# Kernel optimization log

Hardware: AMD Instinct MI355X
Metric: run time of the kernel (lower is better)

Reference implementation:

```python
import jax, jax.numpy as jnp
import numpy as np

D_MODEL = 1024
NHEAD = 16
HEAD_DIM = D_MODEL // NHEAD
B, S = 4, 2048


def setup_inputs() -> dict:
    key = jax.random.key(0)
    ks = jax.random.split(key, 10)
    scale = 1.0 / np.sqrt(D_MODEL)
    inp = {
        "x": jax.random.normal(ks[0], (B, S, D_MODEL), dtype=jnp.float32),
        "y": jax.random.normal(ks[1], (B, S, D_MODEL), dtype=jnp.float32),
        "wq": jax.random.normal(ks[2], (D_MODEL, D_MODEL), dtype=jnp.float32) * scale,
        "bq": jnp.zeros((D_MODEL,), dtype=jnp.float32),
        "wk": jax.random.normal(ks[3], (D_MODEL, D_MODEL), dtype=jnp.float32) * scale,
        "bk": jnp.zeros((D_MODEL,), dtype=jnp.float32),
        "wv": jax.random.normal(ks[4], (D_MODEL, D_MODEL), dtype=jnp.float32) * scale,
        "bv": jnp.zeros((D_MODEL,), dtype=jnp.float32),
        "wo": jax.random.normal(ks[5], (D_MODEL, D_MODEL), dtype=jnp.float32) * scale,
        "bo": jnp.zeros((D_MODEL,), dtype=jnp.float32),
    }
    return inp


def reference(x, y, wq, bq, wk, bk, wv, bv, wo, bo):
    # Linear projections (torch nn.Linear: x @ W.T + b; here weights stored as [in, out])
    q = x @ wq + bq  # [B, S, D]
    k = y @ wk + bk
    v = y @ wv + bv
    # split heads -> [B, H, S, Dh]
    def heads(t):
        return t.reshape(B, S, NHEAD, HEAD_DIM).transpose(0, 2, 1, 3)
    q, k, v = heads(q), heads(k), heads(v)
    scores = jnp.einsum("bhqd,bhkd->bhqk", q, k) / jnp.sqrt(jnp.float32(HEAD_DIM))
    attn = jax.nn.softmax(scores, axis=-1)  # dropout = identity in eval mode
    out = jnp.einsum("bhqk,bhkd->bhqd", attn, v)
    out = out.transpose(0, 2, 1, 3).reshape(B, S, D_MODEL)
    return out @ wo + bo
```

## Files before the change

kernel.cpp:

```cpp
#include <hip/hip_runtime.h>
#include <stdint.h>

#define D_MODEL 1024
#define NHEAD 16
#define HEAD_DIM 64
#define BATCH 4
#define SEQ 2048
#define ROWS (BATCH*SEQ)

typedef __attribute__((ext_vector_type(8))) short short8;
typedef __attribute__((ext_vector_type(4))) float f32x4;
typedef __attribute__((ext_vector_type(2))) unsigned int u32x2;
typedef unsigned short u16;
typedef unsigned int u32;

#define QSCALE 0.18033688011112042f

__device__ __forceinline__ u16 f2b(float f) {
  union { float f; uint32_t u; } in; in.f = f;
  uint32_t u = in.u;
  return (u16)((u + 0x7FFFu + ((u >> 16) & 1u)) >> 16);
}

__device__ __forceinline__ void async_lds16(const void* g, void* l) {
  __builtin_amdgcn_global_load_lds(
      (const __attribute__((address_space(1))) uint32_t*)g,
      (__attribute__((address_space(3))) uint32_t*)l,
      16, 0, 0);
}

__device__ __forceinline__ u32 pack_bf16(float lo, float hi) {
  union { float f; uint32_t u; } a, b; a.f = lo; b.f = hi;
  return __builtin_amdgcn_perm(b.u + 0x8000u, a.u + 0x8000u, 0x07060302u);
}

__global__ void __launch_bounds__(256) cvt_kernel(const float* __restrict__ x,
                                                  const float* __restrict__ y,
                                                  u16* __restrict__ xb,
                                                  u16* __restrict__ yb) {
  const float* in = blockIdx.y ? y : x;
  u16* out = blockIdx.y ? yb : xb;
  int i = blockIdx.x * 256 + threadIdx.x;
  float4 v = ((const float4*)in)[i];
  ushort4 o;
  o.x = f2b(v.x); o.y = f2b(v.y); o.z = f2b(v.z); o.w = f2b(v.w);
  ((ushort4*)out)[i] = o;
}

__global__ void __launch_bounds__(256) wtrans_kernel(const float* __restrict__ wq,
                                                     const float* __restrict__ wk,
                                                     const float* __restrict__ wv,
                                                     const float* __restrict__ wo,
                                                     u16* __restrict__ wtbase) {
  __shared__ u16 tile[64 * 65];
  int z = blockIdx.z;
  const float* w = (z == 0) ? wq : (z == 1 ? wk : (z == 2 ? wv : wo));
  u16* wt = wtbase + (size_t)z * D_MODEL * D_MODEL;
  int t = threadIdx.x;
  int c = t & 63, rb = t >> 6;
  int k0 = blockIdx.x * 64, n0 = blockIdx.y * 64;
#pragma unroll
  for (int i = 0; i < 16; ++i) {
    int r = rb + i * 4;
    tile[c * 65 + r] = f2b(w[(size_t)(k0 + r) * D_MODEL + n0 + c]);
  }
  __syncthreads();
#pragma unroll
  for (int i = 0; i < 16; ++i) {
    int r = rb + i * 4;
    wt[(size_t)(n0 + r) * D_MODEL + k0 + c] = tile[r * 65 + c];
  }
}

template <int MODE>
__device__ __forceinline__ void gemm_bt_core(const u16* __restrict__ A,
                                             const u16* __restrict__ Bt,
                                             const float* __restrict__ bias,
                                             void* __restrict__ Cout, float scale,
                                             int m0, int n0) {
  constexpr int K = 1024, N = 1024;
  constexpr bool SWAP = (MODE != 2);
  __shared__ u16 As[2][128 * 32];
  __shared__ u16 Bs[2][128 * 32];
  int tid = threadIdx.x;
  int wave = tid >> 6, lane = tid & 63;
  int quad = lane >> 4, l16 = lane & 15;
  int wm = wave & 1, wn = wave >> 1;

  f32x4 acc[4][4];
#pragma unroll
  for (int p = 0; p < 4; ++p)
#pragma unroll
    for (int q = 0; q < 4; ++q) acc[p][q] = f32x4{0.f, 0.f, 0.f, 0.f};

  int srow = lane >> 2;
  int scol = (lane & 3) * 16;

  for (int k0 = 0; k0 < K; k0 += 64) {
#pragma unroll
    for (int kh = 0; kh < 2; ++kh) {
#pragma unroll
      for (int i = 0; i < 2; ++i) {
        int c = wave * 2 + i;
        const char* ga = (const char*)(A + (size_t)(m0 + c * 16 + srow) * K + k0 + kh * 32) + scol;
        async_lds16(ga, (char*)As[kh] + c * 1024);
        const char* gb = (const char*)(Bt + (size_t)(n0 + c * 16 + srow) * K + k0 + kh * 32) + scol;
        async_lds16(gb, (char*)Bs[kh] + c * 1024);
      }
    }
    __syncthreads();

#pragma unroll
    for (int kh = 0; kh < 2; ++kh) {
      short8 fa[4], fb[4];
#pragma unroll
      for (int p = 0; p < 4; ++p)
        fa[p] = SWAP
          ? *(const short8*)(Bs[kh] + (wn * 64 + p * 16 + l16) * 32 + quad * 8)
          : *(const short8*)(As[kh] + (wm * 64 + p * 16 + l16) * 32 + quad * 8);
#pragma unroll
      for (int q = 0; q < 4; ++q)
        fb[q] = SWAP
          ? *(const short8*)(As[kh] + (wm * 64 + q * 16 + l16) * 32 + quad * 8)
          : *(const short8*)(Bs[kh] + (wn * 64 + q * 16 + l16) * 32 + quad * 8);
#pragma unroll
      for (int p = 0; p < 4; ++p)
#pragma unroll
        for (int q = 0; q < 4; ++q)
          acc[p][q] = __builtin_amdgcn_mfma_f32_16x16x32_bf16(fa[p], fb[q], acc[p][q], 0, 0, 0);
    }
    __syncthreads();
  }

  if (MODE == 2) {
    int sblk = n0 + wn * 64;
    int bb = sblk >> 11;
    int ssb = sblk & 2047;
#pragma unroll
    for (int p = 0; p < 4; ++p) {
      int dbase = m0 + wm * 64 + p * 16 + quad * 4;
      float4 b4 = *(const float4*)(bias + dbase);
#pragma unroll
      for (int r = 0; r < 4; ++r) {
        int d = dbase + r;
        float bv = ((const float*)&b4)[r];
        u32 lo = pack_bf16(acc[p][0][r] + bv, acc[p][1][r] + bv);
        u32 hi = pack_bf16(acc[p][2][r] + bv, acc[p][3][r] + bv);
        size_t vtrow = ((size_t)bb * 16 + (d >> 6)) * 64 + (d & 63);
        *(u32x2*)((u16*)Cout + vtrow * 2048 + ssb + 4 * l16) = u32x2{lo, hi};
      }
    }
  } else {
#pragma unroll
    for (int p = 0; p < 4; ++p) {
      int nbase = n0 + wn * 64 + p * 16 + quad * 4;
      float4 b4 = *(const float4*)(bias + nbase);
#pragma unroll
      for (int q = 0; q < 4; ++q) {
        size_t mrow = (size_t)(m0 + wm * 64 + q * 16 + l16);
        float v0 = (acc[p][q][0] + b4.x) * scale;
        float v1 = (acc[p][q][1] + b4.y) * scale;
        float v2 = (acc[p][q][2] + b4.z) * scale;
        float v3 = (acc[p][q][3] + b4.w) * scale;
        if (MODE == 1) {
          *(f32x4*)((float*)Cout + mrow * N + nbase) = f32x4{v0, v1, v2, v3};
        } else {
          *(u32x2*)((u16*)Cout + mrow * N + nbase) = u32x2{pack_bf16(v0, v1), pack_bf16(v2, v3)};
        }
      }
    }
  }
}

__global__ void __launch_bounds__(256, 4) gemm_qkv_kernel(
    const u16* __restrict__ xb, const u16* __restrict__ yb,
    const u16* __restrict__ wqT, const u16* __restrict__ wkT, const u16* __restrict__ wvT,
    const float* __restrict__ bq, const float* __restrict__ bk, const float* __restrict__ bv,
    u16* __restrict__ q, u16* __restrict__ k, u16* __restrict__ vt) {
  int bx = blockIdx.x, z = blockIdx.y;
  if (z == 0) {
    gemm_bt_core<0>(xb, wqT, bq, q, QSCALE, (bx >> 3) * 128, (bx & 7) * 128);
  } else if (z == 1) {
    gemm_bt_core<0>(yb, wkT, bk, k, 1.0f, (bx >> 3) * 128, (bx & 7) * 128);
  } else {
    gemm_bt_core<2>(wvT, yb, bv, vt, 1.0f, (bx & 7) * 128, (bx >> 3) * 128);
  }
}

__global__ void __launch_bounds__(256, 4) gemm_o_kernel(const u16* __restrict__ ao,
                                                        const u16* __restrict__ woT,
                                                        const float* __restrict__ bo,
                                                        float* __restrict__ out) {
  gemm_bt_core<1>(ao, woT, bo, out, 1.0f, blockIdx.y * 128, blockIdx.x * 128);
}

__global__ void __launch_bounds__(256, 4) attn_kernel(const u16* __restrict__ Q,
                                                      const u16* __restrict__ Kp,
                                                      const u16* __restrict__ Vt,
                                                      u16* __restrict__ Outp) {
  __shared__ u16 Ks[2][64 * 64];
  __shared__ u16 Vts[2][64 * 64];
  __shared__ u16 Ps[4][16 * 64];

  int tid = threadIdx.x, wave = tid >> 6, lane = tid & 63;
  int quad = lane >> 4, l16 = lane & 15;
  int bh = blockIdx.x;
  int b = bh >> 4, h = bh & 15;
  int q0 = blockIdx.y * 128 + wave * 32;
  size_t gbase = (size_t)b * SEQ * D_MODEL;
  const u16* kbase = Kp + gbase + (size_t)h * HEAD_DIM;
  const u16* vbase = Vt + (size_t)bh * HEAD_DIM * SEQ;
  const u16* qrow = Q + gbase + (size_t)q0 * D_MODEL + (size_t)h * HEAD_DIM;

  short8 aq[2][2];
#pragma unroll
  for (int rs = 0; rs < 2; ++rs)
#pragma unroll
    for (int dc = 0; dc < 2; ++dc)
      aq[rs][dc] = *(const short8*)(qrow + (size_t)(rs * 16 + l16) * D_MODEL + dc * 32 + quad * 8);

  f32x4 Oacc[2][4];
  float lpart[2][4];
#pragma unroll
  for (int rs = 0; rs < 2; ++rs)
#pragma unroll
    for (int ni = 0; ni < 4; ++ni) Oacc[rs][ni] = f32x4{0.f, 0.f, 0.f, 0.f};
#pragma unroll
  for (int rs = 0; rs < 2; ++rs)
#pragma unroll
    for (int r = 0; r < 4; ++r) lpart[rs][r] = 0.f;

  size_t koff[2], voff[2];
  int dstoff[2];
#pragma unroll
  for (int i = 0; i < 2; ++i) {
    int c = i * 256 + tid;
    int krow = c >> 3, kgp = c & 7;
    koff[i] = (size_t)krow * D_MODEL + (size_t)((kgp ^ (krow & 7)) * 8);
    voff[i] = (size_t)krow * SEQ + (size_t)((kgp ^ (krow & 7)) * 8);
    dstoff[i] = i * 4096 + wave * 1024;
  }

#pragma unroll
  for (int i = 0; i < 2; ++i) {
    async_lds16(kbase + koff[i], (char*)Ks[0] + dstoff[i]);
    async_lds16(vbase + voff[i], (char*)Vts[0] + dstoff[i]);
  }

  constexpr int NT = SEQ / 64;
  for (int t = 0; t < NT; ++t) {
    int cur = t & 1;
    __syncthreads();
    if (t + 1 < NT) {
      size_t kvoff = (size_t)(t + 1) * 64;
#pragma unroll
      for (int i = 0; i < 2; ++i) {
        async_lds16(kbase + kvoff * D_MODEL + koff[i], (char*)Ks[cur ^ 1] + dstoff[i]);
        async_lds16(vbase + kvoff + voff[i], (char*)Vts[cur ^ 1] + dstoff[i]);
      }
    }

    const u16* Kc = Ks[cur];
    const u16* Vc = Vts[cur];
    u16* Pw = Ps[wave];
    int x = l16 & 7;

    short8 kf[4][2];
#pragma unroll
    for (int sub = 0; sub < 4; ++sub) {
      const u16* kr = Kc + (sub * 16 + l16) * 64;
      kf[sub][0] = *(const short8*)(kr + ((quad ^ x) << 3));
      kf[sub][1] = *(const short8*)(kr + (((4 + quad) ^ x) << 3));
    }

    short8 pa[2][2];
#pragma unroll
    for (int rs = 0; rs < 2; ++rs) {
      f32x4 S[4];
#pragma unroll
      for (int sub = 0; sub < 4; ++sub) {
        f32x4 s = f32x4{0.f, 0.f, 0.f, 0.f};
        s = __builtin_amdgcn_mfma_f32_16x16x32_bf16(aq[rs][0], kf[sub][0], s, 0, 0, 0);
        s = __builtin_amdgcn_mfma_f32_16x16x32_bf16(aq[rs][1], kf[sub][1], s, 0, 0, 0);
        S[sub] = s;
      }
#pragma unroll
      for (int r = 0; r < 4; ++r) {
        float p0 = __builtin_amdgcn_exp2f(S[0][r]);
        float p1 = __builtin_amdgcn_exp2f(S[1][r]);
        float p2 = __builtin_amdgcn_exp2f(S[2][r]);
        float p3 = __builtin_amdgcn_exp2f(S[3][r]);
        lpart[rs][r] += (p0 + p1) + (p2 + p3);
        u32 lo = pack_bf16(p0, p1);
        u32 hi = pack_bf16(p2, p3);
        int row = quad * 4 + r;
        int off = row * 64 + (((l16 >> 1) ^ (row & 7)) << 3) + ((l16 & 1) << 2);
        *(u32x2*)(Pw + off) = u32x2{lo, hi};
      }
#pragma unroll
      for (int kc = 0; kc < 2; ++kc)
        pa[rs][kc] = *(const short8*)(Pw + l16 * 64 + ((((kc << 2) + quad) ^ x) << 3));
    }

#pragma unroll
    for (int kc = 0; kc < 2; ++kc) {
#pragma unroll
      for (int ni = 0; ni < 4; ++ni) {
        int d = ni * 16 + l16;
        short8 bv = *(const short8*)(Vc + d * 64 + ((((kc << 2) + quad) ^ (l16 & 7)) << 3));
        Oacc[0][ni] = __builtin_amdgcn_mfma_f32_16x16x32_bf16(pa[0][kc], bv, Oacc[0][ni], 0, 0, 0);
        Oacc[1][ni] = __builtin_amdgcn_mfma_f32_16x16x32_bf16(pa[1][kc], bv, Oacc[1][ni], 0, 0, 0);
      }
    }
  }

#pragma unroll
  for (int rs = 0; rs < 2; ++rs)
#pragma unroll
    for (int r = 0; r < 4; ++r) {
      float l = lpart[rs][r];
      l += __shfl_xor(l, 1);
      l += __shfl_xor(l, 2);
      l += __shfl_xor(l, 4);
      l += __shfl_xor(l, 8);
      float inv = 1.0f / l;
      size_t orow = gbase + (size_t)(q0 + rs * 16 + quad * 4 + r) * D_MODEL + (size_t)h * HEAD_DIM;
#pragma unroll
      for (int ni = 0; ni < 4; ++ni)
        Outp[orow + ni * 16 + l16] = f2b(Oacc[rs][ni][r] * inv);
    }
}

extern "C" void kernel_launch(void* const* d_in, const int* in_sizes, int n_in,
                              void* d_out, int out_size, void* d_ws, size_t ws_size,
                              hipStream_t stream) {
  const float* x  = (const float*)d_in[0];
  const float* y  = (const float*)d_in[1];
  const float* wq = (const float*)d_in[2];
  const float* bq = (const float*)d_in[3];
  const float* wk = (const float*)d_in[4];
  const float* bk = (const float*)d_in[5];
  const float* wv = (const float*)d_in[6];
  const float* bv = (const float*)d_in[7];
  const float* wo = (const float*)d_in[8];
  const float* bo = (const float*)d_in[9];
  float* out = (float*)d_out;

  char* ws = (char*)d_ws;
  const size_t SZ_ACT = (size_t)ROWS * D_MODEL * 2;
  const size_t SZ_W   = (size_t)D_MODEL * D_MODEL * 2;
  u16* xb  = (u16*)(ws);
  u16* yb  = (u16*)(ws + SZ_ACT);
  u16* wT  = (u16*)(ws + 2 * SZ_ACT);
  u16* wqT = wT;
  u16* wkT = (u16*)(ws + 2 * SZ_ACT + SZ_W);
  u16* wvT = (u16*)(ws + 2 * SZ_ACT + 2 * SZ_W);
  u16* woT = (u16*)(ws + 2 * SZ_ACT + 3 * SZ_W);
  u16* qb  = (u16*)(ws + 2 * SZ_ACT + 4 * SZ_W);
  u16* kb  = (u16*)(ws + 3 * SZ_ACT + 4 * SZ_W);
  u16* vt  = (u16*)(ws + 4 * SZ_ACT + 4 * SZ_W);
  u16* ao  = (u16*)(ws + 5 * SZ_ACT + 4 * SZ_W);

  cvt_kernel<<<dim3(8192, 2), 256, 0, stream>>>(x, y, xb, yb);
  wtrans_kernel<<<dim3(16, 16, 4), 256, 0, stream>>>(wq, wk, wv, wo, wT);
  gemm_qkv_kernel<<<dim3(512, 3), 256, 0, stream>>>(xb, yb, wqT, wkT, wvT, bq, bk, bv, qb, kb, vt);
  attn_kernel<<<dim3(64, 16), 256, 0, stream>>>(qb, kb, vt, ao);
  gemm_o_kernel<<<dim3(8, 64), 256, 0, stream>>>(ao, woT, bo, out);
}
```

Baseline: 327.6 us.

## Load GEMM and attention MFMA operands directly from global memory, drop LDS staging

Removes the async global-to-LDS double-buffered staging in both the projection GEMM core and the attention kernel. Each lane now reads its MFMA fragments straight from global memory through precomputed row pointers, which removes the __syncthreads barriers and the LDS traffic. In exchange, the reuse of tiles across waves is lost: each wave re-fetches the same K/V and A/B rows through the cache hierarchy, and load latency is no longer hidden by the double buffering. The P tile still goes through per-wave LDS.

```diff
diff --git a/kernel.cpp b/kernel.cpp
--- a/kernel.cpp
+++ b/kernel.cpp
@@ -20,13 +20,6 @@
   union { float f; uint32_t u; } in; in.f = f;
   uint32_t u = in.u;
   return (u16)((u + 0x7FFFu + ((u >> 16) & 1u)) >> 16);
-}
-
-__device__ __forceinline__ void async_lds16(const void* g, void* l) {
-  __builtin_amdgcn_global_load_lds(
-      (const __attribute__((address_space(1))) uint32_t*)g,
-      (__attribute__((address_space(3))) uint32_t*)l,
-      16, 0, 0);
 }
 
 __device__ __forceinline__ u32 pack_bf16(float lo, float hi) {
@@ -80,8 +73,6 @@
                                              int m0, int n0) {
   constexpr int K = 1024, N = 1024;
   constexpr bool SWAP = (MODE != 2);
-  __shared__ u16 As[2][128 * 32];
-  __shared__ u16 Bs[2][128 * 32];
   int tid = threadIdx.x;
   int wave = tid >> 6, lane = tid & 63;
   int quad = lane >> 4, l16 = lane & 15;
@@ -93,43 +84,31 @@
 #pragma unroll
     for (int q = 0; q < 4; ++q) acc[p][q] = f32x4{0.f, 0.f, 0.f, 0.f};
 
-  int srow = lane >> 2;
-  int scol = (lane & 3) * 16;
+  const u16* par[4];
+  const u16* pbr[4];
+#pragma unroll
+  for (int p = 0; p < 4; ++p) {
+    int arow = SWAP ? (n0 + wn * 64 + p * 16 + l16) : (m0 + wm * 64 + p * 16 + l16);
+    int brow = SWAP ? (m0 + wm * 64 + p * 16 + l16) : (n0 + wn * 64 + p * 16 + l16);
+    par[p] = (SWAP ? Bt : A) + (size_t)arow * K + quad * 8;
+    pbr[p] = (SWAP ? A : Bt) + (size_t)brow * K + quad * 8;
+  }
 
   for (int k0 = 0; k0 < K; k0 += 64) {
 #pragma unroll
     for (int kh = 0; kh < 2; ++kh) {
-#pragma unroll
-      for (int i = 0; i < 2; ++i) {
-        int c = wave * 2 + i;
-        const char* ga = (const char*)(A + (size_t)(m0 + c * 16 + srow) * K + k0 + kh * 32) + scol;
-        async_lds16(ga, (char*)As[kh] + c * 1024);
-        const char* gb = (const char*)(Bt + (size_t)(n0 + c * 16 + srow) * K + k0 + kh * 32) + scol;
-        async_lds16(gb, (char*)Bs[kh] + c * 1024);
-      }
-    }
-    __syncthreads();
-
-#pragma unroll
-    for (int kh = 0; kh < 2; ++kh) {
+      int ko = k0 + kh * 32;
       short8 fa[4], fb[4];
 #pragma unroll
-      for (int p = 0; p < 4; ++p)
-        fa[p] = SWAP
-          ? *(const short8*)(Bs[kh] + (wn * 64 + p * 16 + l16) * 32 + quad * 8)
-          : *(const short8*)(As[kh] + (wm * 64 + p * 16 + l16) * 32 + quad * 8);
-#pragma unroll
-      for (int q = 0; q < 4; ++q)
-        fb[q] = SWAP
-          ? *(const short8*)(As[kh] + (wm * 64 + q * 16 + l16) * 32 + quad * 8)
-          : *(const short8*)(Bs[kh] + (wn * 64 + q * 16 + l16) * 32 + quad * 8);
+      for (int p = 0; p < 4; ++p) fa[p] = *(const short8*)(par[p] + ko);
+#pragma unroll
+      for (int q = 0; q < 4; ++q) fb[q] = *(const short8*)(pbr[q] + ko);
 #pragma unroll
       for (int p = 0; p < 4; ++p)
 #pragma unroll
         for (int q = 0; q < 4; ++q)
           acc[p][q] = __builtin_amdgcn_mfma_f32_16x16x32_bf16(fa[p], fb[q], acc[p][q], 0, 0, 0);
     }
-    __syncthreads();
   }
 
   if (MODE == 2) {
@@ -198,8 +177,6 @@
                                                       const u16* __restrict__ Kp,
                                                       const u16* __restrict__ Vt,
                                                       u16* __restrict__ Outp) {
-  __shared__ u16 Ks[2][64 * 64];
-  __shared__ u16 Vts[2][64 * 64];
   __shared__ u16 Ps[4][16 * 64];
 
   int tid = threadIdx.x, wave = tid >> 6, lane = tid & 63;
@@ -230,47 +207,35 @@
 #pragma unroll
     for (int r = 0; r < 4; ++r) lpart[rs][r] = 0.f;
 
-  size_t koff[2], voff[2];
-  int dstoff[2];
-#pragma unroll
-  for (int i = 0; i < 2; ++i) {
-    int c = i * 256 + tid;
-    int krow = c >> 3, kgp = c & 7;
-    koff[i] = (size_t)krow * D_MODEL + (size_t)((kgp ^ (krow & 7)) * 8);
-    voff[i] = (size_t)krow * SEQ + (size_t)((kgp ^ (krow & 7)) * 8);
-    dstoff[i] = i * 4096 + wave * 1024;
-  }
-
-#pragma unroll
-  for (int i = 0; i < 2; ++i) {
-    async_lds16(kbase + koff[i], (char*)Ks[0] + dstoff[i]);
-    async_lds16(vbase + voff[i], (char*)Vts[0] + dstoff[i]);
-  }
-
-  constexpr int NT = SEQ / 64;
-  for (int t = 0; t < NT; ++t) {
-    int cur = t & 1;
-    __syncthreads();
-    if (t + 1 < NT) {
-      size_t kvoff = (size_t)(t + 1) * 64;
-#pragma unroll
-      for (int i = 0; i < 2; ++i) {
-        async_lds16(kbase + kvoff * D_MODEL + koff[i], (char*)Ks[cur ^ 1] + dstoff[i]);
-        async_lds16(vbase + kvoff + voff[i], (char*)Vts[cur ^ 1] + dstoff[i]);
-      }
-    }
-
-    const u16* Kc = Ks[cur];
-    const u16* Vc = Vts[cur];
-    u16* Pw = Ps[wave];
-    int x = l16 & 7;
-
+  const u16* krow[4];
+#pragma unroll
+  for (int sub = 0; sub < 4; ++sub)
+    krow[sub] = kbase + (size_t)(sub * 16 + l16) * D_MODEL + quad * 8;
+  const u16* vrow[4];
+#pragma unroll
+  for (int ni = 0; ni < 4; ++ni)
+    vrow[ni] = vbase + (size_t)(ni * 16 + l16) * SEQ + quad * 8;
+
+  u16* Pw = Ps[wave];
+  int x = l16 & 7;
+  int pwoff[4];
+#pragma unroll
+  for (int r = 0; r < 4; ++r) {
+    int row = quad * 4 + r;
+    pwoff[r] = row * 64 + (((l16 >> 1) ^ (row & 7)) << 3) + ((l16 & 1) << 2);
+  }
+  int paoff[2];
+#pragma unroll
+  for (int kc = 0; kc < 2; ++kc)
+    paoff[kc] = l16 * 64 + ((((kc << 2) + quad) ^ x) << 3);
+
+  for (int kv0 = 0; kv0 < SEQ; kv0 += 64) {
     short8 kf[4][2];
+    size_t kadv = (size_t)kv0 * D_MODEL;
 #pragma unroll
     for (int sub = 0; sub < 4; ++sub) {
-      const u16* kr = Kc + (sub * 16 + l16) * 64;
-      kf[sub][0] = *(const short8*)(kr + ((quad ^ x) << 3));
-      kf[sub][1] = *(const short8*)(kr + (((4 + quad) ^ x) << 3));
+      kf[sub][0] = *(const short8*)(krow[sub] + kadv);
+      kf[sub][1] = *(const short8*)(krow[sub] + kadv + 32);
     }
 
     short8 pa[2][2];
@@ -291,23 +256,18 @@
         float p2 = __builtin_amdgcn_exp2f(S[2][r]);
         float p3 = __builtin_amdgcn_exp2f(S[3][r]);
         lpart[rs][r] += (p0 + p1) + (p2 + p3);
-        u32 lo = pack_bf16(p0, p1);
-        u32 hi = pack_bf16(p2, p3);
-        int row = quad * 4 + r;
-        int off = row * 64 + (((l16 >> 1) ^ (row & 7)) << 3) + ((l16 & 1) << 2);
-        *(u32x2*)(Pw + off) = u32x2{lo, hi};
+        *(u32x2*)(Pw + pwoff[r]) = u32x2{pack_bf16(p0, p1), pack_bf16(p2, p3)};
       }
 #pragma unroll
       for (int kc = 0; kc < 2; ++kc)
-        pa[rs][kc] = *(const short8*)(Pw + l16 * 64 + ((((kc << 2) + quad) ^ x) << 3));
+        pa[rs][kc] = *(const short8*)(Pw + paoff[kc]);
     }
 
 #pragma unroll
     for (int kc = 0; kc < 2; ++kc) {
 #pragma unroll
       for (int ni = 0; ni < 4; ++ni) {
-        int d = ni * 16 + l16;
-        short8 bv = *(const short8*)(Vc + d * 64 + ((((kc << 2) + quad) ^ (l16 & 7)) << 3));
+        short8 bv = *(const short8*)(vrow[ni] + kv0 + (kc << 5));
         Oacc[0][ni] = __builtin_amdgcn_mfma_f32_16x16x32_bf16(pa[0][kc], bv, Oacc[0][ni], 0, 0, 0);
         Oacc[1][ni] = __builtin_amdgcn_mfma_f32_16x16x32_bf16(pa[1][kc], bv, Oacc[1][ni], 0, 0, 0);
       }
```

New measurement: 625.7 us. 91.0% more time.
